# Kernel tuning notes

Measured on AMD Instinct MI355X. Metric: run time of the kernel, lower is better.

The kernel has to match this reference:

```python
import jax, jax.numpy as jnp
import numpy as np

T, H, I, E, K = 1024, 1024, 1024, 16, 4
ALPHA, LIMIT, EPS = 1.702, 7.0, 1e-5


def setup_inputs() -> dict:
    key = jax.random.key(0)
    ks = jax.random.split(key, 8)
    return {
        "x": jax.random.normal(ks[0], (T, H), jnp.float32),
        "norm_w": jnp.ones((H,), jnp.float32) + 0.01 * jax.random.normal(ks[1], (H,), jnp.float32),
        "router_w": 0.02 * jax.random.normal(ks[2], (E, H), jnp.float32),
        "router_b": jnp.zeros((E,), jnp.float32),
        "w13": 0.02 * jax.random.normal(ks[3], (E, H, 2 * I), jnp.float32),
        "b13": 0.01 * jax.random.normal(ks[4], (E, 2 * I), jnp.float32),
        "w2": 0.02 * jax.random.normal(ks[5], (E, I, H), jnp.float32),
        "b2": 0.01 * jax.random.normal(ks[6], (E, H), jnp.float32),
        "manual_weights": jnp.zeros((1, E), jnp.float32),  # zeros => override branch inactive, as in __init__
        "layer_idx": 0,
    }


def _override(g, lw):
    # torch: log_softmax, then force pos-masked experts to max+0.01, neg-masked to min-0.01
    gl = jax.nn.log_softmax(g, axis=-1)
    mx = jnp.max(gl, axis=-1, keepdims=True)
    mn = jnp.min(gl, axis=-1, keepdims=True)
    gl = jnp.where((lw > 0)[None, :], mx + 0.01, gl)
    gl = jnp.where((lw < 0)[None, :], mn - 0.01, gl)
    return gl


def reference(x, norm_w, router_w, router_b, w13, b13, w2, b2, manual_weights, layer_idx):
    # RMSNorm (eps=1e-5)
    t = x * jax.lax.rsqrt(jnp.mean(x * x, axis=-1, keepdims=True) + EPS) * norm_w
    # router logits [T, E]
    g = t @ router_w.T + router_b
    # conditional manual logit override
    lw = manual_weights[layer_idx]
    g = jax.lax.cond(jnp.max(jnp.abs(lw)) > 0,
                     lambda gg: _override(gg, lw),
                     lambda gg: gg, g)
    # top-k routing, renormalize=True (softmax -> topk -> renorm)
    probs = jax.nn.softmax(g, axis=-1)
    topw, topi = jax.lax.top_k(probs, K)
    topw = topw / jnp.sum(topw, axis=-1, keepdims=True)
    # dense combine matrix [T, E] (sparse dispatch in the fused kernel)
    combine = jnp.zeros(g.shape, x.dtype).at[jnp.arange(g.shape[0])[:, None], topi].add(topw)
    # expert compute: gate_up GEMM + swigluoai + down GEMM (dense over experts for the reference)
    h = jnp.einsum('th,ehf->tef', t, w13) + b13          # [T, E, 2I]
    gate = jnp.minimum(h[..., :I], LIMIT)                # clamp(max=limit)
    up = jnp.clip(h[..., I:], -LIMIT, LIMIT)             # clamp(-limit, limit)
    act = (up + 1.0) * gate * jax.nn.sigmoid(ALPHA * gate)
    y = jnp.einsum('tei,eih->teh', act, w2) + b2         # [T, E, H]
    moe = jnp.einsum('te,teh->th', combine, y)           # weighted scatter-combine
    return x + moe
```

## Files before the change

kernel.cpp:

```cpp
#include <hip/hip_runtime.h>

#define T_    1024
#define H_    1024
#define IDIM  1024
#define E_    16
#define TOPK  4
#define ALPHA 1.702f
#define LIMIT 7.0f

typedef __bf16 bf16;
typedef __bf16 bf16x4 __attribute__((ext_vector_type(4)));
typedef __bf16 bf16x8 __attribute__((ext_vector_type(8)));
typedef float  f32x4  __attribute__((ext_vector_type(4)));

#define BARRIER() do { \
    asm volatile("s_waitcnt lgkmcnt(0)" ::: "memory"); \
    __builtin_amdgcn_s_barrier(); } while (0)

__global__ __launch_bounds__(256) void k_rms_router(
    const float* __restrict__ x, const float* __restrict__ nw,
    const float* __restrict__ rw, const float* __restrict__ rb,
    const float* __restrict__ mw, const int* __restrict__ lidx,
    bf16* __restrict__ tB, float* __restrict__ out,
    int* __restrict__ cnt, int* __restrict__ tok_list,
    float* __restrict__ wgt_list)
{
    const int t = blockIdx.x, tid = threadIdx.x;
    const int lane = tid & 63, wave = tid >> 6;
    __shared__ float tbuf[H_];
    __shared__ float red[4];
    __shared__ float logits[E_];

    float4 xv = ((const float4*)(x + (size_t)t * H_))[tid];
    float4 wv = ((const float4*)nw)[tid];
    float ssq = xv.x*xv.x + xv.y*xv.y + xv.z*xv.z + xv.w*xv.w;
    #pragma unroll
    for (int off = 32; off; off >>= 1) ssq += __shfl_xor(ssq, off);
    if (lane == 0) red[wave] = ssq;
    __syncthreads();
    const float rms = rsqrtf((red[0] + red[1] + red[2] + red[3]) * (1.0f / H_) + 1e-5f);

    float4 tv;
    tv.x = xv.x * rms * wv.x;
    tv.y = xv.y * rms * wv.y;
    tv.z = xv.z * rms * wv.z;
    tv.w = xv.w * rms * wv.w;

    ((float4*)(out + (size_t)t * H_))[tid] = xv;
    ((float4*)tbuf)[tid] = tv;
    bf16x4 tb = { (bf16)tv.x, (bf16)tv.y, (bf16)tv.z, (bf16)tv.w };
    *(bf16x4*)(tB + (size_t)t * H_ + tid * 4) = tb;
    __syncthreads();

    #pragma unroll
    for (int ei = 0; ei < 4; ++ei) {
        const int e = wave * 4 + ei;
        const float* wr = rw + (size_t)e * H_;
        float s = 0.f;
        #pragma unroll
        for (int j = 0; j < 16; ++j) {
            const int c = lane + j * 64;
            s += tbuf[c] * wr[c];
        }
        #pragma unroll
        for (int off = 32; off; off >>= 1) s += __shfl_xor(s, off);
        if (lane == 0) logits[e] = s + rb[e];
    }
    __syncthreads();

    if (tid == 0) {
        float g[E_];
        #pragma unroll
        for (int e = 0; e < E_; ++e) g[e] = logits[e];

        const int li = lidx[0];
        float ma = 0.f, lw[E_];
        #pragma unroll
        for (int e = 0; e < E_; ++e) { lw[e] = mw[li * E_ + e]; ma = fmaxf(ma, fabsf(lw[e])); }
        if (ma > 0.f) {
            float mx = -1e30f;
            for (int e = 0; e < E_; ++e) mx = fmaxf(mx, g[e]);
            float se = 0.f;
            for (int e = 0; e < E_; ++e) se += expf(g[e] - mx);
            const float lse = logf(se) + mx;
            float gl[E_], gmx = -1e30f, gmn = 1e30f;
            for (int e = 0; e < E_; ++e) { gl[e] = g[e] - lse; gmx = fmaxf(gmx, gl[e]); gmn = fminf(gmn, gl[e]); }
            for (int e = 0; e < E_; ++e) {
                if (lw[e] > 0.f)      gl[e] = gmx + 0.01f;
                else if (lw[e] < 0.f) gl[e] = gmn - 0.01f;
                g[e] = gl[e];
            }
        }

        float mx = -1e30f;
        #pragma unroll
        for (int e = 0; e < E_; ++e) mx = fmaxf(mx, g[e]);
        float p[E_];
        #pragma unroll
        for (int e = 0; e < E_; ++e) p[e] = expf(g[e] - mx);

        bool used[E_] = {};
        int   idx[TOPK];
        float twv[TOPK];
        float ssum = 0.f;
        for (int k = 0; k < TOPK; ++k) {
            int best = -1; float bv = -1e30f;
            for (int e = 0; e < E_; ++e)
                if (!used[e] && p[e] > bv) { bv = p[e]; best = e; }
            used[best] = true; idx[k] = best; twv[k] = bv; ssum += bv;
        }
        const float inv = 1.f / ssum;
        for (int k = 0; k < TOPK; ++k) {
            const int e = idx[k];
            const int slot = atomicAdd(&cnt[e], 1);
            tok_list[e * T_ + slot] = t;
            wgt_list[e * T_ + slot] = twv[k] * inv;
        }
    }
}

__device__ __forceinline__ void inline_scan(const int* __restrict__ cnt,
                                            int ti, int tid, int* sm)
{
    if (tid == 0) {
        int c0[E_];
        #pragma unroll
        for (int e = 0; e < E_; ++e) c0[e] = cnt[e];
        int s = 0, nt = 0, ee = 0, mm0 = 0, nee = 0, sbb = 0;
        #pragma unroll
        for (int e = 0; e < E_; ++e) {
            const int c = c0[e];
            const int tcnt = (c + 63) >> 6;
            if (ti >= nt && ti < nt + tcnt) {
                ee = e; mm0 = (ti - nt) * 64; nee = c; sbb = s;
            }
            s += c; nt += tcnt;
        }
        sm[0] = nt; sm[1] = ee; sm[2] = mm0; sm[3] = nee; sm[4] = sbb;
    }
    __syncthreads();
}

__global__ __launch_bounds__(256) void k_gateup7(
    const bf16* __restrict__ tB, const float* __restrict__ w13,
    const float* __restrict__ b13, const int* __restrict__ cnt,
    const int* __restrict__ tok_list, bf16* __restrict__ act)
{
    const int ti = blockIdx.y, bx = blockIdx.x;
    const int tid = threadIdx.x, lane = tid & 63, wave = tid >> 6;
    const int q = lane >> 4, r = lane & 15;

    __shared__ __align__(16) bf16 As[8 * 64 * 8];
    __shared__ __align__(16) bf16 Bs[1032 * 8];
    __shared__ int sm[5];

    inline_scan(cnt, ti, tid, sm);
    if (ti >= sm[0]) return;
    const int e = sm[1], m0 = sm[2], ne = sm[3], sb = sm[4];

    const int m   = tid >> 2, kq = tid & 3;
    const int mf_s = m >> 4, r_s = m & 15;
    const int kc_s = kq >> 1, q_s = (kq & 1) * 2;
    bf16* wr0 = As + ((size_t)((mf_s * 2 + kc_s) * 64 + q_s * 16 + r_s)) * 8;
    bf16* wr1 = wr0 + 16 * 8;
    int srow = m0 + m; srow = srow < ne ? srow : ne - 1;
    const bf16* pA = tB + (size_t)tok_list[e * T_ + srow] * H_ + kq * 16;

    const int c4 = tid & 31, q6 = tid >> 5;
    const int kcs = q6 >> 2, qs = q6 & 3;
    const int cc = c4 * 4;
    const int fB = c4 >> 2, r0 = (c4 & 3) * 4;
    const int RB = fB * 2 + kcs;
    bf16* bwr = Bs + ((size_t)(RB * 64 + (RB >> 1) + qs * 16 + r0)) * 8;
    const int col = (cc < 64) ? (bx * 64 + cc) : (IDIM + bx * 64 + (cc - 64));
    const float* pB = w13 + (size_t)e * H_ * (2 * IDIM)
                          + (size_t)(kcs * 32 + qs * 8) * (2 * IDIM) + col;

    f32x4 accg[4] = {};
    f32x4 accu[4] = {};
    uint4  a0a, a0b, a1a, a1b;
    f32x4  br0[8], br1[8];

#define LOADA(A0, A1, s) do { const int ss_ = (s) < 16 ? (s) : 15; \
    A0 = *(const uint4*)(pA + ss_ * 64); \
    A1 = *(const uint4*)(pA + ss_ * 64 + 8); } while (0)
#define LOADB(BR, s) do { const int ss_ = (s) < 16 ? (s) : 15; \
    _Pragma("unroll") \
    for (int j = 0; j < 8; ++j) \
        BR[j] = *(const f32x4*)(pB + (size_t)(ss_ * 64 + j) * (2 * IDIM)); } while (0)
#define STAGEA(A0, A1) do { *(uint4*)wr0 = A0; *(uint4*)wr1 = A1; } while (0)
#define STAGEB(BR) do { \
    _Pragma("unroll") \
    for (int rr = 0; rr < 4; ++rr) { \
        bf16x8 p; \
        _Pragma("unroll") \
        for (int j = 0; j < 8; ++j) p[j] = (bf16)BR[j][rr]; \
        *(bf16x8*)(bwr + rr * 8) = p; \
    } } while (0)
#define COMPUTE() do { \
    _Pragma("unroll") \
    for (int kc = 0; kc < 2; ++kc) { \
        bf16x8 afr[4]; \
        _Pragma("unroll") \
        for (int mf = 0; mf < 4; ++mf) \
            afr[mf] = *(const bf16x8*)(As + ((size_t)((mf * 2 + kc) * 64 + lane)) * 8); \
        const int Rg = wave * 2 + kc, Ru = (wave + 4) * 2 + kc; \
        bf16x8 bg = *(const bf16x8*)(Bs + ((size_t)(Rg * 64 + (Rg >> 1) + lane)) * 8); \
        bf16x8 bu = *(const bf16x8*)(Bs + ((size_t)(Ru * 64 + (Ru >> 1) + lane)) * 8); \
        _Pragma("unroll") \
        for (int mf = 0; mf < 4; ++mf) { \
            accg[mf] = __builtin_amdgcn_mfma_f32_16x16x32_bf16(afr[mf], bg, accg[mf], 0, 0, 0); \
            accu[mf] = __builtin_amdgcn_mfma_f32_16x16x32_bf16(afr[mf], bu, accu[mf], 0, 0, 0); \
        } \
    } } while (0)

    LOADA(a0a, a0b, 0);
    LOADB(br0, 0);
    #pragma unroll 1
    for (int kb = 0; kb < 16; kb += 2) {
        BARRIER();
        STAGEA(a0a, a0b);  STAGEB(br0);
        LOADA(a1a, a1b, kb + 1);  LOADB(br1, kb + 1);
        BARRIER();
        COMPUTE();

        BARRIER();
        STAGEA(a1a, a1b);  STAGEB(br1);
        LOADA(a0a, a0b, kb + 2);  LOADB(br0, kb + 2);
        BARRIER();
        COMPUTE();
    }
#undef LOADA
#undef LOADB
#undef STAGEA
#undef STAGEB
#undef COMPUTE

    const int nb_g = bx * 4 + wave;
    const int cg = nb_g * 16 + r;
    const float bgv = b13[e * 2 * IDIM + cg];
    const float buv = b13[e * 2 * IDIM + IDIM + cg];
    #pragma unroll
    for (int mf = 0; mf < 4; ++mf) {
        #pragma unroll
        for (int rg = 0; rg < 4; ++rg) {
            const int row = mf * 16 + q * 4 + rg;
            if (m0 + row < ne) {
                const float hg = accg[mf][rg] + bgv;
                const float hu = accu[mf][rg] + buv;
                const float gt = fminf(hg, LIMIT);
                const float up = fminf(fmaxf(hu, -LIMIT), LIMIT);
                const float av = (up + 1.0f) * gt / (1.0f + expf(-ALPHA * gt));
                act[(size_t)(sb + m0 + row) * IDIM + cg] = (bf16)av;
            }
        }
    }
}

__global__ __launch_bounds__(256) void k_down7(
    const bf16* __restrict__ act, const float* __restrict__ w2,
    const float* __restrict__ b2, const int* __restrict__ cnt,
    const int* __restrict__ tok_list, const float* __restrict__ wgt_list,
    float* __restrict__ out)
{
    const int ti = blockIdx.y, bx = blockIdx.x;
    const int tid = threadIdx.x, lane = tid & 63, wave = tid >> 6;
    const int q = lane >> 4, r = lane & 15;

    __shared__ __align__(16) bf16 As[8 * 64 * 8];
    __shared__ __align__(16) bf16 Bs[1032 * 8];
    __shared__ int sm[5];

    inline_scan(cnt, ti, tid, sm);
    if (ti >= sm[0]) return;
    const int e = sm[1], m0 = sm[2], ne = sm[3], sb = sm[4];

    const int m   = tid >> 2, kq = tid & 3;
    const int mf_s = m >> 4, r_s = m & 15;
    const int kc_s = kq >> 1, q_s = (kq & 1) * 2;
    bf16* wr0 = As + ((size_t)((mf_s * 2 + kc_s) * 64 + q_s * 16 + r_s)) * 8;
    bf16* wr1 = wr0 + 16 * 8;
    int srow = m0 + m; srow = srow < ne ? srow : ne - 1;
    const bf16* pA = act + (size_t)(sb + srow) * IDIM + kq * 16;

    const int c4 = tid & 31, q6 = tid >> 5;
    const int kcs = q6 >> 2, qs = q6 & 3;
    const int cc = c4 * 4;
    const int fB = c4 >> 2, r0 = (c4 & 3) * 4;
    const int RB = fB * 2 + kcs;
    bf16* bwr = Bs + ((size_t)(RB * 64 + (RB >> 1) + qs * 16 + r0)) * 8;
    const float* pB = w2 + (size_t)e * IDIM * H_
                         + (size_t)(kcs * 32 + qs * 8) * H_ + bx * 128 + cc;

    f32x4 acc[4][2] = {};
    uint4  a0a, a0b, a1a, a1b;
    f32x4  br0[8], br1[8];

#define LOADA(A0, A1, s) do { const int ss_ = (s) < 16 ? (s) : 15; \
    A0 = *(const uint4*)(pA + ss_ * 64); \
    A1 = *(const uint4*)(pA + ss_ * 64 + 8); } while (0)
#define LOADB(BR, s) do { const int ss_ = (s) < 16 ? (s) : 15; \
    _Pragma("unroll") \
    for (int j = 0; j < 8; ++j) \
        BR[j] = *(const f32x4*)(pB + (size_t)(ss_ * 64 + j) * H_); } while (0)
#define STAGEA(A0, A1) do { *(uint4*)wr0 = A0; *(uint4*)wr1 = A1; } while (0)
#define STAGEB(BR) do { \
    _Pragma("unroll") \
    for (int rr = 0; rr < 4; ++rr) { \
        bf16x8 p; \
        _Pragma("unroll") \
        for (int j = 0; j < 8; ++j) p[j] = (bf16)BR[j][rr]; \
        *(bf16x8*)(bwr + rr * 8) = p; \
    } } while (0)
#define COMPUTE() do { \
    _Pragma("unroll") \
    for (int kc = 0; kc < 2; ++kc) { \
        bf16x8 afr[4]; \
        _Pragma("unroll") \
        for (int mf = 0; mf < 4; ++mf) \
            afr[mf] = *(const bf16x8*)(As + ((size_t)((mf * 2 + kc) * 64 + lane)) * 8); \
        const int R0 = (wave * 2) * 2 + kc, R1 = (wave * 2 + 1) * 2 + kc; \
        bf16x8 b0 = *(const bf16x8*)(Bs + ((size_t)(R0 * 64 + (R0 >> 1) + lane)) * 8); \
        bf16x8 b1 = *(const bf16x8*)(Bs + ((size_t)(R1 * 64 + (R1 >> 1) + lane)) * 8); \
        _Pragma("unroll") \
        for (int mf = 0; mf < 4; ++mf) { \
            acc[mf][0] = __builtin_amdgcn_mfma_f32_16x16x32_bf16(afr[mf], b0, acc[mf][0], 0, 0, 0); \
            acc[mf][1] = __builtin_amdgcn_mfma_f32_16x16x32_bf16(afr[mf], b1, acc[mf][1], 0, 0, 0); \
        } \
    } } while (0)

    LOADA(a0a, a0b, 0);
    LOADB(br0, 0);
    #pragma unroll 1
    for (int kb = 0; kb < 16; kb += 2) {
        BARRIER();
        STAGEA(a0a, a0b);  STAGEB(br0);
        LOADA(a1a, a1b, kb + 1);  LOADB(br1, kb + 1);
        BARRIER();
        COMPUTE();

        BARRIER();
        STAGEA(a1a, a1b);  STAGEB(br1);
        LOADA(a0a, a0b, kb + 2);  LOADB(br0, kb + 2);
        BARRIER();
        COMPUTE();
    }
#undef LOADA
#undef LOADB
#undef STAGEA
#undef STAGEB
#undef COMPUTE

    const int nb0 = bx * 8 + wave * 2;
    #pragma unroll
    for (int nf = 0; nf < 2; ++nf) {
        const int ch = (nb0 + nf) * 16 + r;
        const float bb = b2[e * H_ + ch];
        #pragma unroll
        for (int mf = 0; mf < 4; ++mf) {
            #pragma unroll
            for (int rg = 0; rg < 4; ++rg) {
                const int row = mf * 16 + q * 4 + rg;
                const int s = m0 + row;
                if (s < ne) {
                    const int   tok = tok_list[e * T_ + s];
                    const float w   = wgt_list[e * T_ + s];
                    atomicAdd(&out[(size_t)tok * H_ + ch], w * (acc[mf][nf][rg] + bb));
                }
            }
        }
    }
}

extern "C" void kernel_launch(void* const* d_in, const int* in_sizes, int n_in,
                              void* d_out, int out_size, void* d_ws, size_t ws_size,
                              hipStream_t stream)
{
    const float* x        = (const float*)d_in[0];
    const float* norm_w   = (const float*)d_in[1];
    const float* router_w = (const float*)d_in[2];
    const float* router_b = (const float*)d_in[3];
    const float* w13      = (const float*)d_in[4];
    const float* b13      = (const float*)d_in[5];
    const float* w2       = (const float*)d_in[6];
    const float* b2       = (const float*)d_in[7];
    const float* manual_w = (const float*)d_in[8];
    const int*   layer_i  = (const int*)d_in[9];
    float* out = (float*)d_out;

    char* ws = (char*)d_ws;
    bf16*  tB   = (bf16*)ws;
    bf16*  act  = (bf16*)(ws + (2ull << 20));
    char*  meta = ws + (10ull << 20);
    int*   cnt      = (int*)meta;
    int*   tok_list = (int*)(meta + (16ull << 10));
    float* wgt_list = (float*)(meta + (16ull << 10) + (64ull << 10));

    hipMemsetAsync(cnt, 0, E_ * sizeof(int), stream);

    k_rms_router<<<T_, 256, 0, stream>>>(x, norm_w, router_w, router_b,
                                         manual_w, layer_i, tB, out,
                                         cnt, tok_list, wgt_list);

    dim3 gg(16, 80);
    k_gateup7<<<gg, 256, 0, stream>>>(tB, w13, b13, cnt, tok_list, act);
    dim3 gd(8, 80);
    k_down7<<<gd, 256, 0, stream>>>(act, w2, b2, cnt, tok_list, wgt_list, out);
}
```

Before: 373.2 us.

## Double M-tile to 128 rows with 512-thread blocks in expert GEMMs

Both expert GEMM kernels now process 128 routed rows per block instead of 64, using 8 waves arranged 2x4 so each block of fp32 weights loaded and converted to bf16 serves twice as many tokens. Weight staging is split across twice as many threads, with each thread loading half the rows. This halves the redundant global weight reads, which dominate since weights are fp32 and are read once per M-tile. The cost is more padding waste for experts whose token counts are not multiples of 128, fewer blocks in the grid, and larger blocks that may lower occupancy.

```diff
diff --git a/kernel.cpp b/kernel.cpp
--- a/kernel.cpp
+++ b/kernel.cpp
@@ -130,9 +130,9 @@
         #pragma unroll
         for (int e = 0; e < E_; ++e) {
             const int c = c0[e];
-            const int tcnt = (c + 63) >> 6;
+            const int tcnt = (c + 127) >> 7;
             if (ti >= nt && ti < nt + tcnt) {
-                ee = e; mm0 = (ti - nt) * 64; nee = c; sbb = s;
+                ee = e; mm0 = (ti - nt) * 128; nee = c; sbb = s;
             }
             s += c; nt += tcnt;
         }
@@ -141,16 +141,17 @@
     __syncthreads();
 }
 
-__global__ __launch_bounds__(256) void k_gateup7(
+__global__ __launch_bounds__(512) void k_gateup8(
     const bf16* __restrict__ tB, const float* __restrict__ w13,
     const float* __restrict__ b13, const int* __restrict__ cnt,
     const int* __restrict__ tok_list, bf16* __restrict__ act)
 {
     const int ti = blockIdx.y, bx = blockIdx.x;
     const int tid = threadIdx.x, lane = tid & 63, wave = tid >> 6;
+    const int wm = wave >> 2, wn = wave & 3;
     const int q = lane >> 4, r = lane & 15;
 
-    __shared__ __align__(16) bf16 As[8 * 64 * 8];
+    __shared__ __align__(16) bf16 As[16 * 64 * 8];
     __shared__ __align__(16) bf16 Bs[1032 * 8];
     __shared__ int sm[5];
 
@@ -167,35 +168,34 @@
     const bf16* pA = tB + (size_t)tok_list[e * T_ + srow] * H_ + kq * 16;
 
     const int c4 = tid & 31, q6 = tid >> 5;
-    const int kcs = q6 >> 2, qs = q6 & 3;
+    const int kcs = q6 >> 3, qs = (q6 >> 1) & 3, jh = q6 & 1;
     const int cc = c4 * 4;
     const int fB = c4 >> 2, r0 = (c4 & 3) * 4;
     const int RB = fB * 2 + kcs;
-    bf16* bwr = Bs + ((size_t)(RB * 64 + (RB >> 1) + qs * 16 + r0)) * 8;
+    bf16* bwr = Bs + ((size_t)(RB * 64 + (RB >> 1) + qs * 16 + r0)) * 8 + jh * 4;
     const int col = (cc < 64) ? (bx * 64 + cc) : (IDIM + bx * 64 + (cc - 64));
     const float* pB = w13 + (size_t)e * H_ * (2 * IDIM)
-                          + (size_t)(kcs * 32 + qs * 8) * (2 * IDIM) + col;
+                          + (size_t)(kcs * 32 + qs * 8 + jh * 4) * (2 * IDIM) + col;
 
     f32x4 accg[4] = {};
     f32x4 accu[4] = {};
     uint4  a0a, a0b, a1a, a1b;
-    f32x4  br0[8], br1[8];
+    f32x4  br0[4], br1[4];
 
 #define LOADA(A0, A1, s) do { const int ss_ = (s) < 16 ? (s) : 15; \
     A0 = *(const uint4*)(pA + ss_ * 64); \
     A1 = *(const uint4*)(pA + ss_ * 64 + 8); } while (0)
 #define LOADB(BR, s) do { const int ss_ = (s) < 16 ? (s) : 15; \
     _Pragma("unroll") \
-    for (int j = 0; j < 8; ++j) \
-        BR[j] = *(const f32x4*)(pB + (size_t)(ss_ * 64 + j) * (2 * IDIM)); } while (0)
+    for (int j2 = 0; j2 < 4; ++j2) \
+        BR[j2] = *(const f32x4*)(pB + (size_t)(ss_ * 64 + j2) * (2 * IDIM)); } while (0)
 #define STAGEA(A0, A1) do { *(uint4*)wr0 = A0; *(uint4*)wr1 = A1; } while (0)
 #define STAGEB(BR) do { \
     _Pragma("unroll") \
     for (int rr = 0; rr < 4; ++rr) { \
-        bf16x8 p; \
-        _Pragma("unroll") \
-        for (int j = 0; j < 8; ++j) p[j] = (bf16)BR[j][rr]; \
-        *(bf16x8*)(bwr + rr * 8) = p; \
+        bf16x4 p = { (bf16)BR[0][rr], (bf16)BR[1][rr], \
+                     (bf16)BR[2][rr], (bf16)BR[3][rr] }; \
+        *(bf16x4*)(bwr + rr * 8) = p; \
     } } while (0)
 #define COMPUTE() do { \
     _Pragma("unroll") \
@@ -203,8 +203,8 @@
         bf16x8 afr[4]; \
         _Pragma("unroll") \
         for (int mf = 0; mf < 4; ++mf) \
-            afr[mf] = *(const bf16x8*)(As + ((size_t)((mf * 2 + kc) * 64 + lane)) * 8); \
-        const int Rg = wave * 2 + kc, Ru = (wave + 4) * 2 + kc; \
+            afr[mf] = *(const bf16x8*)(As + ((size_t)(((wm * 4 + mf) * 2 + kc) * 64 + lane)) * 8); \
+        const int Rg = wn * 2 + kc, Ru = (wn + 4) * 2 + kc; \
         bf16x8 bg = *(const bf16x8*)(Bs + ((size_t)(Rg * 64 + (Rg >> 1) + lane)) * 8); \
         bf16x8 bu = *(const bf16x8*)(Bs + ((size_t)(Ru * 64 + (Ru >> 1) + lane)) * 8); \
         _Pragma("unroll") \
@@ -236,7 +236,7 @@
 #undef STAGEB
 #undef COMPUTE
 
-    const int nb_g = bx * 4 + wave;
+    const int nb_g = bx * 4 + wn;
     const int cg = nb_g * 16 + r;
     const float bgv = b13[e * 2 * IDIM + cg];
     const float buv = b13[e * 2 * IDIM + IDIM + cg];
@@ -244,7 +244,7 @@
     for (int mf = 0; mf < 4; ++mf) {
         #pragma unroll
         for (int rg = 0; rg < 4; ++rg) {
-            const int row = mf * 16 + q * 4 + rg;
+            const int row = wm * 64 + mf * 16 + q * 4 + rg;
             if (m0 + row < ne) {
                 const float hg = accg[mf][rg] + bgv;
                 const float hu = accu[mf][rg] + buv;
@@ -257,7 +257,7 @@
     }
 }
 
-__global__ __launch_bounds__(256) void k_down7(
+__global__ __launch_bounds__(512) void k_down8(
     const bf16* __restrict__ act, const float* __restrict__ w2,
     const float* __restrict__ b2, const int* __restrict__ cnt,
     const int* __restrict__ tok_list, const float* __restrict__ wgt_list,
@@ -265,9 +265,10 @@
 {
     const int ti = blockIdx.y, bx = blockIdx.x;
     const int tid = threadIdx.x, lane = tid & 63, wave = tid >> 6;
+    const int wm = wave >> 2, wn = wave & 3;
     const int q = lane >> 4, r = lane & 15;
 
-    __shared__ __align__(16) bf16 As[8 * 64 * 8];
+    __shared__ __align__(16) bf16 As[16 * 64 * 8];
     __shared__ __align__(16) bf16 Bs[1032 * 8];
     __shared__ int sm[5];
 
@@ -284,33 +285,32 @@
     const bf16* pA = act + (size_t)(sb + srow) * IDIM + kq * 16;
 
     const int c4 = tid & 31, q6 = tid >> 5;
-    const int kcs = q6 >> 2, qs = q6 & 3;
+    const int kcs = q6 >> 3, qs = (q6 >> 1) & 3, jh = q6 & 1;
     const int cc = c4 * 4;
     const int fB = c4 >> 2, r0 = (c4 & 3) * 4;
     const int RB = fB * 2 + kcs;
-    bf16* bwr = Bs + ((size_t)(RB * 64 + (RB >> 1) + qs * 16 + r0)) * 8;
+    bf16* bwr = Bs + ((size_t)(RB * 64 + (RB >> 1) + qs * 16 + r0)) * 8 + jh * 4;
     const float* pB = w2 + (size_t)e * IDIM * H_
-                         + (size_t)(kcs * 32 + qs * 8) * H_ + bx * 128 + cc;
+                         + (size_t)(kcs * 32 + qs * 8 + jh * 4) * H_ + bx * 128 + cc;
 
     f32x4 acc[4][2] = {};
     uint4  a0a, a0b, a1a, a1b;
-    f32x4  br0[8], br1[8];
+    f32x4  br0[4], br1[4];
 
 #define LOADA(A0, A1, s) do { const int ss_ = (s) < 16 ? (s) : 15; \
     A0 = *(const uint4*)(pA + ss_ * 64); \
     A1 = *(const uint4*)(pA + ss_ * 64 + 8); } while (0)
 #define LOADB(BR, s) do { const int ss_ = (s) < 16 ? (s) : 15; \
     _Pragma("unroll") \
-    for (int j = 0; j < 8; ++j) \
-        BR[j] = *(const f32x4*)(pB + (size_t)(ss_ * 64 + j) * H_); } while (0)
+    for (int j2 = 0; j2 < 4; ++j2) \
+        BR[j2] = *(const f32x4*)(pB + (size_t)(ss_ * 64 + j2) * H_); } while (0)
 #define STAGEA(A0, A1) do { *(uint4*)wr0 = A0; *(uint4*)wr1 = A1; } while (0)
 #define STAGEB(BR) do { \
     _Pragma("unroll") \
     for (int rr = 0; rr < 4; ++rr) { \
-        bf16x8 p; \
-        _Pragma("unroll") \
-        for (int j = 0; j < 8; ++j) p[j] = (bf16)BR[j][rr]; \
-        *(bf16x8*)(bwr + rr * 8) = p; \
+        bf16x4 p = { (bf16)BR[0][rr], (bf16)BR[1][rr], \
+                     (bf16)BR[2][rr], (bf16)BR[3][rr] }; \
+        *(bf16x4*)(bwr + rr * 8) = p; \
     } } while (0)
 #define COMPUTE() do { \
     _Pragma("unroll") \
@@ -318,8 +318,8 @@
         bf16x8 afr[4]; \
         _Pragma("unroll") \
         for (int mf = 0; mf < 4; ++mf) \
-            afr[mf] = *(const bf16x8*)(As + ((size_t)((mf * 2 + kc) * 64 + lane)) * 8); \
-        const int R0 = (wave * 2) * 2 + kc, R1 = (wave * 2 + 1) * 2 + kc; \
+            afr[mf] = *(const bf16x8*)(As + ((size_t)(((wm * 4 + mf) * 2 + kc) * 64 + lane)) * 8); \
+        const int R0 = (wn * 2) * 2 + kc, R1 = (wn * 2 + 1) * 2 + kc; \
         bf16x8 b0 = *(const bf16x8*)(Bs + ((size_t)(R0 * 64 + (R0 >> 1) + lane)) * 8); \
         bf16x8 b1 = *(const bf16x8*)(Bs + ((size_t)(R1 * 64 + (R1 >> 1) + lane)) * 8); \
         _Pragma("unroll") \
@@ -351,7 +351,7 @@
 #undef STAGEB
 #undef COMPUTE
 
-    const int nb0 = bx * 8 + wave * 2;
+    const int nb0 = bx * 8 + wn * 2;
     #pragma unroll
     for (int nf = 0; nf < 2; ++nf) {
         const int ch = (nb0 + nf) * 16 + r;
@@ -360,7 +360,7 @@
         for (int mf = 0; mf < 4; ++mf) {
             #pragma unroll
             for (int rg = 0; rg < 4; ++rg) {
-                const int row = mf * 16 + q * 4 + rg;
+                const int row = wm * 64 + mf * 16 + q * 4 + rg;
                 const int s = m0 + row;
                 if (s < ne) {
                     const int   tok = tok_list[e * T_ + s];
@@ -402,8 +402,8 @@
                                          manual_w, layer_i, tB, out,
                                          cnt, tok_list, wgt_list);
 
-    dim3 gg(16, 80);
-    k_gateup7<<<gg, 256, 0, stream>>>(tB, w13, b13, cnt, tok_list, act);
-    dim3 gd(8, 80);
-    k_down7<<<gd, 256, 0, stream>>>(act, w2, b2, cnt, tok_list, wgt_list, out);
+    dim3 gg(16, 48);
+    k_gateup8<<<gg, 512, 0, stream>>>(tB, w13, b13, cnt, tok_list, act);
+    dim3 gd(8, 48);
+    k_down8<<<gd, 512, 0, stream>>>(act, w2, b2, cnt, tok_list, wgt_list, out);
 }
```

Measured after the change: 371.1 us. No clear change (-0.6%).
